# Optimization experiments

Measured on AMD Instinct MI355X. Metric: run time of the kernel, lower is better.

Reference implementation:

```python
import jax, jax.numpy as jnp
import numpy as np
import math

_PHI = (1.0 + 5.0 ** 0.5) / 2.0
_VERTS_RAW = np.array([(-1, _PHI, 0), (1, _PHI, 0), (-1, -_PHI, 0), (1, -_PHI, 0),
                       (0, -1, _PHI), (0, 1, _PHI), (0, -1, -_PHI), (0, 1, -_PHI),
                       (_PHI, 0, -1), (_PHI, 0, 1), (-_PHI, 0, -1), (-_PHI, 0, 1)], dtype=np.float32)
_VERTS = _VERTS_RAW / np.linalg.norm(_VERTS_RAW, axis=1, keepdims=True)
_FACES = [(0,11,5),(0,5,1),(0,1,7),(0,7,10),(0,10,11),(1,5,9),(5,11,4),(11,10,2),(10,7,6),(7,1,8),
          (3,9,4),(3,4,2),(3,2,6),(3,6,8),(3,8,9),(4,9,5),(2,4,11),(6,2,10),(8,6,7),(9,8,1)]

def _build_edges():
    es = set()
    for f in _FACES:
        for i in range(3):
            es.add(tuple(sorted((f[i], f[(i + 1) % 3]))))
    return np.array(sorted(es), dtype=np.int32)

_EDGES = _build_edges()  # [30, 2] undirected edges of the icosahedron


def _grid_mapping(lat, lon):
    # Mirrors IcosahedralFlowMatch._grid_mapping exactly (incl. the view/permute quirk).
    lat_c = jnp.linspace(-math.pi / 2, math.pi / 2, lat)
    lon_c = jnp.linspace(-math.pi, math.pi, lon)
    lon_g, lat_g = jnp.meshgrid(lon_c, lat_c, indexing='xy')  # each [lat, lon]
    flat = jnp.stack([lat_g, lon_g], axis=-1).reshape(-1, 2)  # [G, 2]
    verts = jnp.asarray(_VERTS)
    vlat = jnp.arcsin(verts[:, 2])
    vlon = jnp.arctan2(verts[:, 1], verts[:, 0])
    dlat = flat[None, :, 0] - vlat[:, None]
    dlon = jnp.remainder(flat[None, :, 1] - vlon[:, None] + math.pi, 2 * math.pi) - math.pi
    d2 = dlat ** 2 + dlon ** 2                            # [12, G]
    vert_to_grid = jnp.argmin(d2, axis=1)                 # [12] nearest grid cell per vertex
    grid_to_vert = jnp.argmin(d2, axis=0)                 # [G] nearest vertex per grid cell
    grid_to_vert = grid_to_vert.reshape(lon, lat).T       # torch: .view(lon,lat).permute(1,0)
    return vert_to_grid, grid_to_vert


def setup_inputs() -> dict:
    key = jax.random.key(0)
    ks = jax.random.split(key, 8)
    B, C, H, W = 16, 4, 721, 1440
    D, L = 256, 4
    s = 0.02
    return {
        'x': jax.random.normal(ks[0], (B, C, H, W), jnp.float32),
        't': jax.random.uniform(ks[1], (B,), dtype=jnp.float32),
        'W_in': jax.random.normal(ks[2], (C, D), jnp.float32) * s,
        'b_in': jnp.zeros((D,), jnp.float32),
        'W_layers': jax.random.normal(ks[3], (L, D, D), jnp.float32) * s,
        'b_layers': jax.random.normal(ks[4], (L, D), jnp.float32) * s,
        'W_out': jax.random.normal(ks[5], (D, C), jnp.float32) * s,
        'b_out': jnp.zeros((C,), jnp.float32),
    }


def reference(x, t, W_in, b_in, W_layers, b_layers, W_out, b_out):
    B, C, H, W = x.shape
    v2g, g2v = _grid_mapping(H, W)
    nodes = x.transpose(0, 2, 3, 1).reshape(B, H * W, C)   # [B, G, C]
    feats = nodes[:, v2g, :]                               # [B, 12, C] gather vertex features
    hn = feats @ W_in + b_in                               # [B, 12, D]
    src = jnp.asarray(_EDGES[:, 0])
    dst = jnp.asarray(_EDGES[:, 1])
    n_verts = _VERTS.shape[0]
    deg = jnp.zeros((n_verts,), hn.dtype).at[dst].add(1.0).at[src].add(1.0)
    deg = jnp.maximum(deg, 1.0)[None, :, None]
    for i in range(W_layers.shape[0]):                     # fixed n_layers=4
        agg = jnp.zeros_like(hn).at[:, dst, :].add(hn[:, src, :]).at[:, src, :].add(hn[:, dst, :])
        agg = agg / deg
        hn = hn + jax.nn.relu(agg @ W_layers[i] + b_layers[i])
    out_nodes = hn @ W_out + b_out                         # [B, 12, C]
    out = out_nodes[:, g2v.reshape(-1), :].reshape(B, H, W, C).transpose(0, 3, 1, 2)
    return out
```

## Files before the change

### kernel.cpp

```cpp
#include <hip/hip_runtime.h>
#include <math.h>

#define HH 721
#define WW 1440
#define HWV (HH*WW)
#define NB 16
#define NC 4
#define ND 256
#define NL 4
#define NQ (HWV/4)

#define PHI_F 1.61803398874989484820458683436564f

#define WS_V2G 0
#define WS_VLL 64
#define WS_TBL 512
#define WS_HNA 4096
#define WS_HNB (4096 + NB*12*ND*4)

typedef float vfloat4 __attribute__((ext_vector_type(4)));

__constant__ float c_rx[12] = {-1.f, 1.f, -1.f, 1.f,  0.f, 0.f, 0.f, 0.f,
                               PHI_F, PHI_F, -PHI_F, -PHI_F};
__constant__ float c_ry[12] = {PHI_F, PHI_F, -PHI_F, -PHI_F, -1.f, 1.f, -1.f, 1.f,
                               0.f, 0.f, 0.f, 0.f};
__constant__ float c_rz[12] = {0.f, 0.f, 0.f, 0.f, PHI_F, PHI_F, -PHI_F, -PHI_F,
                               -1.f, 1.f, -1.f, 1.f};
__constant__ int c_nbr[12][5] = {
    {11, 5, 1, 7, 10}, {0, 5, 7, 9, 8}, {11, 10, 3, 4, 6}, {9, 4, 2, 6, 8},
    {5, 11, 3, 9, 2},  {0, 11, 1, 9, 4}, {10, 7, 3, 2, 8}, {0, 1, 10, 6, 8},
    {7, 1, 3, 6, 9},   {1, 5, 3, 4, 8},  {0, 7, 11, 2, 6}, {0, 5, 10, 4, 2}};

__device__ __forceinline__ void vert_latlon(int v, double* olat, double* olon) {
#pragma clang fp contract(off)
  const float P = PHI_F;
  float n = sqrtf(1.0f + P * P);
  float xf = c_rx[v] / n;
  float yf = c_ry[v] / n;
  float zf = c_rz[v] / n;
  *olat = asin((double)zf);
  *olon = atan2((double)yf, (double)xf);
}

__device__ __forceinline__ double grid_lat(int i) {
#pragma clang fp contract(off)
  if (i == 720) return M_PI / 2;
  double v = (double)i * (M_PI / 720.0);
  return v - M_PI / 2;
}

__device__ __forceinline__ double grid_lon(int j) {
#pragma clang fp contract(off)
  if (j == 1439) return M_PI;
  double v = (double)j * (2.0 * M_PI / 1439.0);
  return v - M_PI;
}

__device__ __forceinline__ double d2f(double lat, double lon, double vlat,
                                      double vlon) {
#pragma clang fp contract(off)
  double dlat = lat - vlat;
  double x = (lon - vlon) + M_PI;
  const double TP = 2.0 * M_PI;
  double r = (x < 0.0) ? (x + TP) : ((x >= TP) ? (x - TP) : x);
  double dlon = r - M_PI;
  return dlat * dlat + dlon * dlon;
}

__global__ __launch_bounds__(64) void map_kernel(char* __restrict__ ws) {
  const int t = threadIdx.x;
  if (t >= 12) return;
  int* v2g = (int*)(ws + WS_V2G);
  double* vll = (double*)(ws + WS_VLL);
  double vlat, vlon;
  vert_latlon(t, &vlat, &vlon);
  vll[t] = vlat;
  vll[12 + t] = vlon;
  int i0 = (int)floor((vlat + M_PI / 2) / (M_PI / 720.0) + 0.5);
  int j0 = (int)floor((vlon + M_PI) / (2.0 * M_PI / 1439.0) + 0.5);
  int cand[11] = {0, 1, 2, 1437, 1438, 1439, j0 - 2, j0 - 1, j0, j0 + 1, j0 + 2};
  for (int a = 6; a < 11; a++) {
    if (cand[a] < 0) cand[a] = 0;
    if (cand[a] > 1439) cand[a] = 1439;
  }
  for (int a = 1; a < 11; a++) {
    int key = cand[a];
    int p = a - 1;
    while (p >= 0 && cand[p] > key) {
      cand[p + 1] = cand[p];
      p--;
    }
    cand[p + 1] = key;
  }
  double best = 1e300;
  int bi = 0;
  for (int ii = i0 - 2; ii <= i0 + 2; ii++) {
    if (ii < 0 || ii > 720) continue;
    double lat = grid_lat(ii);
    int prev = -1;
    for (int a = 0; a < 11; a++) {
      int j = cand[a];
      if (j == prev) continue;
      prev = j;
      double dq = d2f(lat, grid_lon(j), vlat, vlon);
      if (dq < best) {
        best = dq;
        bi = ii * 1440 + j;
      }
    }
  }
  v2g[t] = bi;
}

__global__ __launch_bounds__(256) void init_kernel(
    const float* __restrict__ x, const float* __restrict__ W_in,
    const float* __restrict__ b_in, char* __restrict__ ws) {
  __shared__ float s_f[4];
  const int blk = blockIdx.x;
  const int b = blk / 12, n = blk % 12;
  const int t = threadIdx.x;
  const int* v2g = (const int*)(ws + WS_V2G);
  float* hnA = (float*)(ws + WS_HNA);
  if (t < 4) s_f[t] = x[(size_t)(b * NC + t) * HWV + v2g[n]];
  __syncthreads();
  float s = b_in[t];
#pragma unroll
  for (int c = 0; c < 4; c++) s += s_f[c] * W_in[c * ND + t];
  hnA[(size_t)(b * 12 + n) * ND + t] = s;
}

__global__ __launch_bounds__(256) void layer_kernel(
    const float* __restrict__ hsrc, float* __restrict__ hdst,
    const float* __restrict__ Wl, const float* __restrict__ bl,
    const float* __restrict__ W_out, const float* __restrict__ b_out,
    float* __restrict__ tbl, int do_out) {
  __shared__ float s_agg[ND];
  __shared__ float s_hn[ND];
  const int blk = blockIdx.x;
  const int b = blk / 12, n = blk % 12;
  const int t = threadIdx.x;

  float a = 0.f;
#pragma unroll
  for (int e = 0; e < 5; e++)
    a += hsrc[(size_t)(b * 12 + c_nbr[n][e]) * ND + t];
  s_agg[t] = a / 5.0f;
  float hold = hsrc[(size_t)(b * 12 + n) * ND + t];
  __syncthreads();

  float acc = 0.f;
  const float* W = Wl + t;
#pragma unroll 8
  for (int dd = 0; dd < ND; dd += 4) {
    vfloat4 a4 = *(const vfloat4*)&s_agg[dd];
    float w0 = W[(size_t)(dd + 0) * ND];
    float w1 = W[(size_t)(dd + 1) * ND];
    float w2 = W[(size_t)(dd + 2) * ND];
    float w3 = W[(size_t)(dd + 3) * ND];
    acc += a4.x * w0; acc += a4.y * w1; acc += a4.z * w2; acc += a4.w * w3;
  }
  float u = acc + bl[t];
  float hnew = hold + ((u > 0.f) ? u : 0.f);
  hdst[(size_t)(b * 12 + n) * ND + t] = hnew;

  if (do_out) {
    s_hn[t] = hnew;
    __syncthreads();
    if (t < 4) {
      int c = t;
      float s = b_out[c];
      for (int dd = 0; dd < ND; dd++) s += s_hn[dd] * W_out[dd * 4 + c];
      tbl[b * 48 + c * 12 + n] = s;
    }
  }
}

__global__ __launch_bounds__(256) void scatter_kernel(
    const char* __restrict__ ws, float* __restrict__ out) {
  __shared__ float s_tbl[NB * NC * 12];
  __shared__ double svlat[12], svlon[12];
  const int t = threadIdx.x;
  const double* vll = (const double*)(ws + WS_VLL);
  const float* tbl_g = (const float*)(ws + WS_TBL);
  if (t < 12) {
    svlat[t] = vll[t];
    svlon[t] = vll[12 + t];
  }
  for (int i = t; i < NB * NC * 12; i += 256) s_tbl[i] = tbl_g[i];
  __syncthreads();

  int q = blockIdx.x * 256 + t;
  if (q >= NQ) return;
  int h = q / 360;
  int w4 = (q - h * 360) * 4;

  int v[4];
#pragma unroll
  for (int s2 = 0; s2 < 4; s2++) {
    int kk = (w4 + s2) * 721 + h;
    int i2 = kk / 1440;
    int j2 = kk - i2 * 1440;
    double lat = grid_lat(i2);
    double lon = grid_lon(j2);
    double best = 1e300;
    int bv = 0;
#pragma unroll
    for (int vv = 0; vv < 12; vv++) {
      double dd = d2f(lat, lon, svlat[vv], svlon[vv]);
      if (dd < best) {
        best = dd;
        bv = vv;
      }
    }
    if (i2 == 360 && bv >= 8) bv ^= 1;
    v[s2] = bv;
  }

  vfloat4* out4 = (vfloat4*)out;
#pragma unroll
  for (int b = 0; b < NB; b++) {
#pragma unroll
    for (int c = 0; c < NC; c++) {
      const float* tb = &s_tbl[b * 48 + c * 12];
      vfloat4 val = {tb[v[0]], tb[v[1]], tb[v[2]], tb[v[3]]};
      __builtin_nontemporal_store(val, &out4[(size_t)(b * 4 + c) * NQ + q]);
    }
  }
}

extern "C" void kernel_launch(void* const* d_in, const int* in_sizes, int n_in,
                              void* d_out, int out_size, void* d_ws,
                              size_t ws_size, hipStream_t stream) {
  const float* x = (const float*)d_in[0];
  const float* W_in = (const float*)d_in[2];
  const float* b_in = (const float*)d_in[3];
  const float* W_layers = (const float*)d_in[4];
  const float* b_layers = (const float*)d_in[5];
  const float* W_out = (const float*)d_in[6];
  const float* b_out = (const float*)d_in[7];
  float* out = (float*)d_out;
  char* ws = (char*)d_ws;
  float* tbl = (float*)(ws + WS_TBL);
  float* hnA = (float*)(ws + WS_HNA);
  float* hnB = (float*)(ws + WS_HNB);

  map_kernel<<<1, 64, 0, stream>>>(ws);
  init_kernel<<<NB * 12, 256, 0, stream>>>(x, W_in, b_in, ws);
  const float* hs = hnA;
  float* hd = hnB;
  for (int l = 0; l < NL; l++) {
    layer_kernel<<<NB * 12, 256, 0, stream>>>(
        hs, hd, W_layers + (size_t)l * ND * ND, b_layers + (size_t)l * ND,
        W_out, b_out, tbl, (l == NL - 1) ? 1 : 0);
    const float* tmp = hd;
    hd = (float*)hs;
    hs = tmp;
  }
  int blocks = (NQ + 255) / 256;
  scatter_kernel<<<blocks, 256, 0, stream>>>(ws, out);
}
```

Baseline: 442.9 us.

## Fuse GNN map, init and layer kernels into one cooperative grid-synced kernel

Replaces the map, init and four per-layer launches with a single cooperative kernel that uses grid-wide syncs between layers. Each block computes its vertex's nearest grid cell inline, and the scatter kernel recomputes vertex lat/lon itself instead of reading them from workspace. This removes several tiny kernel launches and the gaps between them. The cost is cooperative-launch overhead and grid barrier latency. The whole GNN part is small compared with the roughly 265 MB output scatter.

```diff
diff --git a/kernel.cpp b/kernel.cpp
--- a/kernel.cpp
+++ b/kernel.cpp
@@ -1,5 +1,8 @@
 #include <hip/hip_runtime.h>
+#include <hip/hip_cooperative_groups.h>
 #include <math.h>
+
+namespace cg = cooperative_groups;
 
 #define HH 721
 #define WW 1440
@@ -12,8 +15,6 @@
 
 #define PHI_F 1.61803398874989484820458683436564f
 
-#define WS_V2G 0
-#define WS_VLL 64
 #define WS_TBL 512
 #define WS_HNA 4096
 #define WS_HNB (4096 + NB*12*ND*4)
@@ -67,15 +68,9 @@
   return dlat * dlat + dlon * dlon;
 }
 
-__global__ __launch_bounds__(64) void map_kernel(char* __restrict__ ws) {
-  const int t = threadIdx.x;
-  if (t >= 12) return;
-  int* v2g = (int*)(ws + WS_V2G);
-  double* vll = (double*)(ws + WS_VLL);
+__device__ __forceinline__ int v2g_argmin(int n) {
   double vlat, vlon;
-  vert_latlon(t, &vlat, &vlon);
-  vll[t] = vlat;
-  vll[12 + t] = vlon;
+  vert_latlon(n, &vlat, &vlon);
   int i0 = (int)floor((vlat + M_PI / 2) / (M_PI / 720.0) + 0.5);
   int j0 = (int)floor((vlon + M_PI) / (2.0 * M_PI / 1439.0) + 0.5);
   int cand[11] = {0, 1, 2, 1437, 1438, 1439, j0 - 2, j0 - 1, j0, j0 + 1, j0 + 2};
@@ -109,82 +104,93 @@
       }
     }
   }
-  v2g[t] = bi;
-}
-
-__global__ __launch_bounds__(256) void init_kernel(
+  return bi;
+}
+
+__global__ __launch_bounds__(256) void gnn_fused(
     const float* __restrict__ x, const float* __restrict__ W_in,
-    const float* __restrict__ b_in, char* __restrict__ ws) {
+    const float* __restrict__ b_in, const float* __restrict__ W_layers,
+    const float* __restrict__ b_layers, const float* __restrict__ W_out,
+    const float* __restrict__ b_out, char* __restrict__ ws) {
   __shared__ float s_f[4];
+  __shared__ float s_agg[ND];
+  __shared__ float s_hn[ND];
+  __shared__ int s_k;
   const int blk = blockIdx.x;
   const int b = blk / 12, n = blk % 12;
   const int t = threadIdx.x;
-  const int* v2g = (const int*)(ws + WS_V2G);
   float* hnA = (float*)(ws + WS_HNA);
-  if (t < 4) s_f[t] = x[(size_t)(b * NC + t) * HWV + v2g[n]];
+  float* hnB = (float*)(ws + WS_HNB);
+  float* tbl = (float*)(ws + WS_TBL);
+
+  if (t == 0) s_k = v2g_argmin(n);
   __syncthreads();
-  float s = b_in[t];
-#pragma unroll
-  for (int c = 0; c < 4; c++) s += s_f[c] * W_in[c * ND + t];
-  hnA[(size_t)(b * 12 + n) * ND + t] = s;
-}
-
-__global__ __launch_bounds__(256) void layer_kernel(
-    const float* __restrict__ hsrc, float* __restrict__ hdst,
-    const float* __restrict__ Wl, const float* __restrict__ bl,
-    const float* __restrict__ W_out, const float* __restrict__ b_out,
-    float* __restrict__ tbl, int do_out) {
-  __shared__ float s_agg[ND];
-  __shared__ float s_hn[ND];
-  const int blk = blockIdx.x;
-  const int b = blk / 12, n = blk % 12;
-  const int t = threadIdx.x;
-
-  float a = 0.f;
-#pragma unroll
-  for (int e = 0; e < 5; e++)
-    a += hsrc[(size_t)(b * 12 + c_nbr[n][e]) * ND + t];
-  s_agg[t] = a / 5.0f;
-  float hold = hsrc[(size_t)(b * 12 + n) * ND + t];
+  if (t < 4) s_f[t] = x[(size_t)(b * NC + t) * HWV + s_k];
   __syncthreads();
 
-  float acc = 0.f;
-  const float* W = Wl + t;
+  {
+    float s = b_in[t];
+#pragma unroll
+    for (int c = 0; c < 4; c++) s += s_f[c] * W_in[c * ND + t];
+    hnA[(size_t)(b * 12 + n) * ND + t] = s;
+  }
+  cg::this_grid().sync();
+
+  const float* hs = hnA;
+  float* hd = hnB;
+  for (int l = 0; l < NL; l++) {
+    float a = 0.f;
+#pragma unroll
+    for (int e = 0; e < 5; e++)
+      a += hs[(size_t)(b * 12 + c_nbr[n][e]) * ND + t];
+    s_agg[t] = a / 5.0f;
+    float hold = hs[(size_t)(b * 12 + n) * ND + t];
+    __syncthreads();
+
+    float acc = 0.f;
+    const float* W = W_layers + (size_t)l * ND * ND + t;
 #pragma unroll 8
-  for (int dd = 0; dd < ND; dd += 4) {
-    vfloat4 a4 = *(const vfloat4*)&s_agg[dd];
-    float w0 = W[(size_t)(dd + 0) * ND];
-    float w1 = W[(size_t)(dd + 1) * ND];
-    float w2 = W[(size_t)(dd + 2) * ND];
-    float w3 = W[(size_t)(dd + 3) * ND];
-    acc += a4.x * w0; acc += a4.y * w1; acc += a4.z * w2; acc += a4.w * w3;
-  }
-  float u = acc + bl[t];
-  float hnew = hold + ((u > 0.f) ? u : 0.f);
-  hdst[(size_t)(b * 12 + n) * ND + t] = hnew;
-
-  if (do_out) {
-    s_hn[t] = hnew;
-    __syncthreads();
-    if (t < 4) {
-      int c = t;
-      float s = b_out[c];
-      for (int dd = 0; dd < ND; dd++) s += s_hn[dd] * W_out[dd * 4 + c];
-      tbl[b * 48 + c * 12 + n] = s;
+    for (int dd = 0; dd < ND; dd += 4) {
+      vfloat4 a4 = *(const vfloat4*)&s_agg[dd];
+      float w0 = W[(size_t)(dd + 0) * ND];
+      float w1 = W[(size_t)(dd + 1) * ND];
+      float w2 = W[(size_t)(dd + 2) * ND];
+      float w3 = W[(size_t)(dd + 3) * ND];
+      acc += a4.x * w0; acc += a4.y * w1; acc += a4.z * w2; acc += a4.w * w3;
+    }
+    float u = acc + b_layers[l * ND + t];
+    float hnew = hold + ((u > 0.f) ? u : 0.f);
+
+    if (l < NL - 1) {
+      hd[(size_t)(b * 12 + n) * ND + t] = hnew;
+      cg::this_grid().sync();
+      const float* tmp = hd;
+      hd = (float*)hs;
+      hs = tmp;
+      __syncthreads();
+    } else {
+      s_hn[t] = hnew;
+      __syncthreads();
+      if (t < 4) {
+        int c = t;
+        float s = b_out[c];
+        for (int dd = 0; dd < ND; dd++) s += s_hn[dd] * W_out[dd * 4 + c];
+        tbl[b * 48 + c * 12 + n] = s;
+      }
     }
   }
 }
 
 __global__ __launch_bounds__(256) void scatter_kernel(
-    const char* __restrict__ ws, float* __restrict__ out) {
+    const float* __restrict__ tbl_g, float* __restrict__ out) {
   __shared__ float s_tbl[NB * NC * 12];
   __shared__ double svlat[12], svlon[12];
   const int t = threadIdx.x;
-  const double* vll = (const double*)(ws + WS_VLL);
-  const float* tbl_g = (const float*)(ws + WS_TBL);
   if (t < 12) {
-    svlat[t] = vll[t];
-    svlon[t] = vll[12 + t];
+    double a, o;
+    vert_latlon(t, &a, &o);
+    svlat[t] = a;
+    svlon[t] = o;
   }
   for (int i = t; i < NB * NC * 12; i += 256) s_tbl[i] = tbl_g[i];
   __syncthreads();
@@ -241,21 +247,13 @@
   float* out = (float*)d_out;
   char* ws = (char*)d_ws;
   float* tbl = (float*)(ws + WS_TBL);
-  float* hnA = (float*)(ws + WS_HNA);
-  float* hnB = (float*)(ws + WS_HNB);
-
-  map_kernel<<<1, 64, 0, stream>>>(ws);
-  init_kernel<<<NB * 12, 256, 0, stream>>>(x, W_in, b_in, ws);
-  const float* hs = hnA;
-  float* hd = hnB;
-  for (int l = 0; l < NL; l++) {
-    layer_kernel<<<NB * 12, 256, 0, stream>>>(
-        hs, hd, W_layers + (size_t)l * ND * ND, b_layers + (size_t)l * ND,
-        W_out, b_out, tbl, (l == NL - 1) ? 1 : 0);
-    const float* tmp = hd;
-    hd = (float*)hs;
-    hs = tmp;
-  }
+
+  void* args[] = {(void*)&x,        (void*)&W_in,  (void*)&b_in,
+                  (void*)&W_layers, (void*)&b_layers, (void*)&W_out,
+                  (void*)&b_out,    (void*)&ws};
+  hipLaunchCooperativeKernel((const void*)gnn_fused, dim3(NB * 12), dim3(256),
+                             args, 0, stream);
+
   int blocks = (NQ + 255) / 256;
-  scatter_kernel<<<blocks, 256, 0, stream>>>(ws, out);
-}
+  scatter_kernel<<<blocks, 256, 0, stream>>>(tbl, out);
+}
```

Measured after the change: 538.4 us. 1.22x slower.
